# Kernel tuning notes

Hardware: AMD Instinct MI355X
Metric: run time of the kernel (lower is better)

## Reference

```python
import jax, jax.numpy as jnp
import numpy as np

NUM_EXPERTS = 8
TOP_K = 2
D = 1024


def setup_inputs() -> dict:
    key = jax.random.key(0)
    ks = jax.random.split(key, 5)
    T = 16384
    x = jax.random.normal(ks[0], (T, D), dtype=jnp.float32)
    # torch nn.Linear params: weight [out, in], bias [out]
    Wg = jax.random.normal(ks[1], (NUM_EXPERTS, D), dtype=jnp.float32) * (1.0 / np.sqrt(D))
    bg = jnp.zeros((NUM_EXPERTS,), dtype=jnp.float32)
    We = jax.random.normal(ks[2], (NUM_EXPERTS, D, D), dtype=jnp.float32) * (1.0 / np.sqrt(D))
    be = jax.random.normal(ks[3], (NUM_EXPERTS, D), dtype=jnp.float32) * 0.01
    return {"x": x, "Wg": Wg, "bg": bg, "We": We, "be": be}


def reference(x, Wg, bg, We, be):
    T = x.shape[0]
    # gate logits [T, E]
    gate_logits = x @ Wg.T + bg
    top_k_gates, top_k_idx = jax.lax.top_k(gate_logits, TOP_K)  # [T, K]
    top_k_gates = jax.nn.softmax(top_k_gates, axis=-1)
    # dense per-expert combine weight: sum of gate probs where idx == e
    combine = jnp.zeros((T, NUM_EXPERTS), dtype=x.dtype)
    combine = combine.at[jnp.arange(T)[:, None], top_k_idx].add(top_k_gates)  # [T, E]
    # all-expert dense matmul (faithful to the original naive loop): [E, T, out]
    expert_out = jnp.einsum('td,eod->eto', x, We) + be[:, None, :]
    # weighted combine: output[t] = sum_e combine[t,e] * expert_out[e,t]
    out = jnp.einsum('te,eto->to', combine, expert_out)
    return out
```

## Files before the change

kernel.cpp:

```cpp
#include <hip/hip_runtime.h>
#include <hip/hip_bf16.h>
#include <stdint.h>

#define DDIM 1024
#define NEXP 8
#define SEG  16384

typedef __attribute__((ext_vector_type(8))) short bf16x8;
typedef __attribute__((ext_vector_type(4))) float f32x4;
typedef __attribute__((ext_vector_type(8))) unsigned short u16x8;

__device__ __forceinline__ unsigned short f2bf(float f) {
    union { float f; unsigned int u; } v; v.f = f;
    unsigned int u = v.u;
    return (unsigned short)((u + 0x7FFFu + ((u >> 16) & 1u)) >> 16);
}
__device__ __forceinline__ float bf2f(unsigned short h) {
    union { unsigned int u; float f; } v; v.u = ((unsigned int)h) << 16;
    return v.f;
}

__global__ __launch_bounds__(512) void prep(
    const float* __restrict__ x, const float* __restrict__ Wg,
    const float* __restrict__ bg, const float* __restrict__ We,
    unsigned short* __restrict__ xb, unsigned short* __restrict__ web,
    int* __restrict__ cnt, int* __restrict__ tok_list,
    float* __restrict__ gate_list) {

    __shared__ int   se[64];
    __shared__ float sg[64];

    if (blockIdx.x >= 512) {
        size_t idx = ((size_t)(blockIdx.x - 512) * 512 + threadIdx.x) * 8;
        const f32x4* p = (const f32x4*)(We + idx);
        f32x4 a = __builtin_nontemporal_load(p);
        f32x4 b = __builtin_nontemporal_load(p + 1);
        u16x8 h;
        h[0] = f2bf(a[0]); h[1] = f2bf(a[1]); h[2] = f2bf(a[2]); h[3] = f2bf(a[3]);
        h[4] = f2bf(b[0]); h[5] = f2bf(b[1]); h[6] = f2bf(b[2]); h[7] = f2bf(b[3]);
        *(u16x8*)(web + idx) = h;
        return;
    }

    int wave = threadIdx.x >> 6, lane = threadIdx.x & 63;
    int tbase = blockIdx.x * 32;

#pragma unroll
    for (int i = 0; i < 4; i++) {
        int lt = wave * 4 + i;
        int t = tbase + lt;
        const float* xr = x + (size_t)t * DDIM;
        int c0 = lane * 16;

        float4 v[4];
#pragma unroll
        for (int j = 0; j < 4; j++) v[j] = ((const float4*)(xr + c0))[j];

        u16x8 h0, h1;
        h0[0] = f2bf(v[0].x); h0[1] = f2bf(v[0].y); h0[2] = f2bf(v[0].z); h0[3] = f2bf(v[0].w);
        h0[4] = f2bf(v[1].x); h0[5] = f2bf(v[1].y); h0[6] = f2bf(v[1].z); h0[7] = f2bf(v[1].w);
        h1[0] = f2bf(v[2].x); h1[1] = f2bf(v[2].y); h1[2] = f2bf(v[2].z); h1[3] = f2bf(v[2].w);
        h1[4] = f2bf(v[3].x); h1[5] = f2bf(v[3].y); h1[6] = f2bf(v[3].z); h1[7] = f2bf(v[3].w);
        u16x8* xo = (u16x8*)(xb + (size_t)t * DDIM + c0);
        xo[0] = h0; xo[1] = h1;

        float acc[NEXP];
#pragma unroll
        for (int e = 0; e < NEXP; e++) {
            const float4* wg = (const float4*)(Wg + e * DDIM + c0);
            float s = 0.f;
#pragma unroll
            for (int j = 0; j < 4; j++) {
                float4 w = wg[j];
                s += v[j].x * w.x + v[j].y * w.y + v[j].z * w.z + v[j].w * w.w;
            }
            acc[e] = s;
        }
#pragma unroll
        for (int e = 0; e < NEXP; e++) {
#pragma unroll
            for (int o = 32; o > 0; o >>= 1) acc[e] += __shfl_xor(acc[e], o, 64);
        }

        if (lane == 0) {
            float l1 = -1e30f, l2 = -1e30f; int e1 = 0, e2 = 0;
#pragma unroll
            for (int e = 0; e < NEXP; e++) {
                float le = acc[e] + bg[e];
                if (le > l1) { l2 = l1; e2 = e1; l1 = le; e1 = e; }
                else if (le > l2) { l2 = le; e2 = e; }
            }
            float g1 = 1.0f / (1.0f + __expf(l2 - l1));
            float g2 = 1.0f - g1;
            se[lt * 2]     = e1; sg[lt * 2]     = g1;
            se[lt * 2 + 1] = e2; sg[lt * 2 + 1] = g2;
        }
    }
    __syncthreads();

    if (threadIdx.x < NEXP) {
        int e = threadIdx.x;
        int k = 0;
#pragma unroll 8
        for (int i = 0; i < 64; i++) k += (se[i] == e);
        if (k) {
            int p = atomicAdd(cnt + e, k);
            for (int i = 0; i < 64; i++) {
                if (se[i] == e) {
                    tok_list[e * SEG + p]  = (tbase + (i >> 1)) * 2 + (i & 1);
                    gate_list[e * SEG + p] = sg[i];
                    p++;
                }
            }
        }
    }
}

template<bool STORE>
__global__ __launch_bounds__(256, 3) void moe_gemm(
    const unsigned short* __restrict__ xb, const unsigned short* __restrict__ web,
    const float* __restrict__ be, const int* __restrict__ cnt,
    const int* __restrict__ tok_list, const float* __restrict__ gate_list,
    unsigned short* __restrict__ Sb, float* __restrict__ outa) {

    int id = blockIdx.y, e = 0, c = 0;
    while (e < NEXP) {
        c = cnt[e];
        int mt = (c + 127) >> 7;
        if (id < mt) break;
        id -= mt; e++;
    }
    if (e == NEXP) return;
    int m0 = id << 7;
    int n0 = blockIdx.x << 7;

    __shared__ __align__(16) unsigned short lAB[16384];
    unsigned short* lA = lAB;
    unsigned short* lB = lAB + 8192;
    __shared__ int   tok_s[128];
    __shared__ float gate_s[128];

    int tid = threadIdx.x;
    int wave = tid >> 6, lane = tid & 63;

    if (tid < 128) {
        int r = m0 + tid;
        int rc = min(r, c - 1);
        tok_s[tid]  = tok_list[e * SEG + rc];
        gate_s[tid] = (r < c) ? gate_list[e * SEG + rc] : 0.0f;
    }
    __syncthreads();

    int rsub = lane >> 3;
    int gsrc = (lane & 7) ^ rsub;

    const unsigned short* agp[4];
    const unsigned short* bgp[4];
#pragma unroll
    for (int j = 0; j < 4; j++) {
        int row = (wave * 4 + j) * 8 + rsub;
        agp[j] = xb + (size_t)(tok_s[row] >> 1) * DDIM + gsrc * 8;
        bgp[j] = web + ((size_t)e << 20) + (size_t)(n0 + row) * DDIM + gsrc * 8;
    }

    f32x4 acc[4][4];
    f32x4 zz = {0.f, 0.f, 0.f, 0.f};
#pragma unroll
    for (int mi = 0; mi < 4; mi++)
#pragma unroll
        for (int ni = 0; ni < 4; ni++) acc[mi][ni] = zz;

    int wm = (wave >> 1) * 64;
    int wn = (wave & 1) * 64;
    int mrow = lane & 15;
    int q = lane >> 4;

    int offA[4], swA[4], offB[4], swB[4];
#pragma unroll
    for (int i = 0; i < 4; i++) {
        int ra = wm + i * 16 + mrow;
        offA[i] = ra * 64; swA[i] = ra & 7;
        int rb = wn + i * 16 + mrow;
        offB[i] = rb * 64; swB[i] = rb & 7;
    }

    for (int kt = 0; kt < 16; kt++) {
        int k0 = kt * 64;
#pragma unroll
        for (int j = 0; j < 4; j++) {
            __builtin_amdgcn_global_load_lds(
                (const __attribute__((address_space(1))) void*)(agp[j] + k0),
                (__attribute__((address_space(3))) void*)(&lA[(wave * 4 + j) * 512]),
                16, 0, 0);
            __builtin_amdgcn_global_load_lds(
                (const __attribute__((address_space(1))) void*)(bgp[j] + k0),
                (__attribute__((address_space(3))) void*)(&lB[(wave * 4 + j) * 512]),
                16, 0, 0);
        }
        __syncthreads();
#pragma unroll
        for (int kh = 0; kh < 2; kh++) {
            int gq = kh * 4 + q;
            bf16x8 af[4], bfr[4];
#pragma unroll
            for (int i = 0; i < 4; i++)
                af[i] = *(const bf16x8*)&lA[offA[i] + ((gq ^ swA[i]) << 3)];
#pragma unroll
            for (int i = 0; i < 4; i++)
                bfr[i] = *(const bf16x8*)&lB[offB[i] + ((gq ^ swB[i]) << 3)];
#pragma unroll
            for (int mi = 0; mi < 4; mi++)
#pragma unroll
                for (int ni = 0; ni < 4; ni++)
                    acc[mi][ni] = __builtin_amdgcn_mfma_f32_16x16x32_bf16(
                        af[mi], bfr[ni], acc[mi][ni], 0, 0, 0);
        }
        __syncthreads();
    }

    if (STORE) {
#pragma unroll
        for (int ni = 0; ni < 4; ni++) {
            int col = wn + ni * 16 + mrow;
            float bias = be[e * DDIM + n0 + col];
            int cg = col >> 3, cl = col & 7;
#pragma unroll
            for (int mi = 0; mi < 4; mi++) {
#pragma unroll
                for (int r = 0; r < 4; r++) {
                    int row = wm + mi * 16 + q * 4 + r;
                    float vv = gate_s[row] * (acc[mi][ni][r] + bias);
                    lAB[row * 128 + ((cg ^ (row & 7)) << 3) + cl] = f2bf(vv);
                }
            }
        }
        __syncthreads();
#pragma unroll
        for (int j = 0; j < 8; j++) {
            int t = j * 256 + tid;
            int row = t >> 4, gc = t & 15;
            u16x8 vv = *(const u16x8*)&lAB[row * 128 + ((gc ^ (row & 7)) << 3)];
            if (m0 + row < c)
                *(u16x8*)(Sb + (size_t)tok_s[row] * DDIM + n0 + gc * 8) = vv;
        }
    } else {
#pragma unroll
        for (int ni = 0; ni < 4; ni++) {
            int col = n0 + wn + ni * 16 + mrow;
            float bias = be[e * DDIM + col];
#pragma unroll
            for (int mi = 0; mi < 4; mi++) {
#pragma unroll
                for (int r = 0; r < 4; r++) {
                    int rl = wm + mi * 16 + q * 4 + r;
                    if (m0 + rl < c) {
                        float g = gate_s[rl];
                        atomicAdd(outa + (size_t)(tok_s[rl] >> 1) * DDIM + col,
                                  g * (acc[mi][ni][r] + bias));
                    }
                }
            }
        }
    }
}

__global__ void combine(const unsigned short* __restrict__ S, float* __restrict__ out) {
    size_t i = (size_t)blockIdx.x * 256 + threadIdx.x;
    size_t t = i >> 7;
    size_t g = i & 127;
    const u16x8* r0 = (const u16x8*)(S + t * 2 * DDIM) + g;
    const u16x8* r1 = (const u16x8*)(S + (t * 2 + 1) * DDIM) + g;
    u16x8 a = *r0;
    u16x8 b = *r1;
    f32x4 o0, o1;
#pragma unroll
    for (int k = 0; k < 4; k++) o0[k] = bf2f(a[k]) + bf2f(b[k]);
#pragma unroll
    for (int k = 0; k < 4; k++) o1[k] = bf2f(a[4 + k]) + bf2f(b[4 + k]);
    f32x4* op = (f32x4*)(out + t * DDIM + g * 8);
    __builtin_nontemporal_store(o0, op);
    __builtin_nontemporal_store(o1, op + 1);
}

extern "C" void kernel_launch(void* const* d_in, const int* in_sizes, int n_in,
                              void* d_out, int out_size, void* d_ws, size_t ws_size,
                              hipStream_t stream) {
    const float* x  = (const float*)d_in[0];
    const float* Wg = (const float*)d_in[1];
    const float* bg = (const float*)d_in[2];
    const float* We = (const float*)d_in[3];
    const float* be = (const float*)d_in[4];
    float* out = (float*)d_out;

    char* ws = (char*)d_ws;
    unsigned short* xb  = (unsigned short*)ws;
    unsigned short* web = (unsigned short*)(ws + 33554432);
    int*   tok_list  = (int*)(ws + 33554432 + 16777216);
    float* gate_list = (float*)(ws + 33554432 + 16777216 + 524288);
    int*   cnt       = (int*)(ws + 33554432 + 16777216 + 1048576);
    unsigned short* S = (unsigned short*)(ws + 52428800);

    const size_t NEED = 52428800ull + (size_t)32768 * DDIM * 2;

    hipMemsetAsync(cnt, 0, NEXP * sizeof(int), stream);

    prep<<<2560, 512, 0, stream>>>(x, Wg, bg, We, xb, web, cnt, tok_list, gate_list);

    if (ws_size >= NEED) {
        moe_gemm<true><<<dim3(8, 264), 256, 0, stream>>>(
            xb, web, be, cnt, tok_list, gate_list, S, nullptr);
        combine<<<8192, 256, 0, stream>>>(S, out);
    } else {
        hipMemsetAsync(d_out, 0, (size_t)out_size * sizeof(float), stream);
        moe_gemm<false><<<dim3(8, 264), 256, 0, stream>>>(
            xb, web, be, cnt, tok_list, gate_list, nullptr, out);
    }
}
```

Before: 306.1 us.

## Use 128x256 tiles with triple-buffered LDS pipeline in MoE GEMM

Reworks the expert GEMM to use 128x256 output tiles, with each wave computing 128x64, and K-steps of 32. A three-stage LDS ring buffer in dynamic shared memory lets global loads for step k+2 overlap the MFMA work on step k, synchronised by vmcnt waits and barriers instead of two __syncthreads per step. It also adds s_setprio around MFMAs and changes the prep kernel's x/Wg access to a half-row-split layout. The cost is more accumulator registers (occupancy bound drops from 3 to 2 blocks) and 72KB of LDS per block.

```diff
diff --git a/kernel.cpp b/kernel.cpp
--- a/kernel.cpp
+++ b/kernel.cpp
@@ -50,30 +50,33 @@
         int lt = wave * 4 + i;
         int t = tbase + lt;
         const float* xr = x + (size_t)t * DDIM;
-        int c0 = lane * 16;
-
-        float4 v[4];
-#pragma unroll
-        for (int j = 0; j < 4; j++) v[j] = ((const float4*)(xr + c0))[j];
+        int c0 = lane * 8;
+
+        float4 v0 = ((const float4*)(xr + c0))[0];
+        float4 v1 = ((const float4*)(xr + c0))[1];
+        float4 v2 = ((const float4*)(xr + c0 + 512))[0];
+        float4 v3 = ((const float4*)(xr + c0 + 512))[1];
 
         u16x8 h0, h1;
-        h0[0] = f2bf(v[0].x); h0[1] = f2bf(v[0].y); h0[2] = f2bf(v[0].z); h0[3] = f2bf(v[0].w);
-        h0[4] = f2bf(v[1].x); h0[5] = f2bf(v[1].y); h0[6] = f2bf(v[1].z); h0[7] = f2bf(v[1].w);
-        h1[0] = f2bf(v[2].x); h1[1] = f2bf(v[2].y); h1[2] = f2bf(v[2].z); h1[3] = f2bf(v[2].w);
-        h1[4] = f2bf(v[3].x); h1[5] = f2bf(v[3].y); h1[6] = f2bf(v[3].z); h1[7] = f2bf(v[3].w);
-        u16x8* xo = (u16x8*)(xb + (size_t)t * DDIM + c0);
-        xo[0] = h0; xo[1] = h1;
+        h0[0] = f2bf(v0.x); h0[1] = f2bf(v0.y); h0[2] = f2bf(v0.z); h0[3] = f2bf(v0.w);
+        h0[4] = f2bf(v1.x); h0[5] = f2bf(v1.y); h0[6] = f2bf(v1.z); h0[7] = f2bf(v1.w);
+        h1[0] = f2bf(v2.x); h1[1] = f2bf(v2.y); h1[2] = f2bf(v2.z); h1[3] = f2bf(v2.w);
+        h1[4] = f2bf(v3.x); h1[5] = f2bf(v3.y); h1[6] = f2bf(v3.z); h1[7] = f2bf(v3.w);
+        *(u16x8*)(xb + (size_t)t * DDIM + c0) = h0;
+        *(u16x8*)(xb + (size_t)t * DDIM + c0 + 512) = h1;
 
         float acc[NEXP];
 #pragma unroll
         for (int e = 0; e < NEXP; e++) {
-            const float4* wg = (const float4*)(Wg + e * DDIM + c0);
-            float s = 0.f;
-#pragma unroll
-            for (int j = 0; j < 4; j++) {
-                float4 w = wg[j];
-                s += v[j].x * w.x + v[j].y * w.y + v[j].z * w.z + v[j].w * w.w;
-            }
+            const float* wr = Wg + e * DDIM;
+            float4 w0 = ((const float4*)(wr + c0))[0];
+            float4 w1 = ((const float4*)(wr + c0))[1];
+            float4 w2 = ((const float4*)(wr + c0 + 512))[0];
+            float4 w3 = ((const float4*)(wr + c0 + 512))[1];
+            float s = v0.x*w0.x + v0.y*w0.y + v0.z*w0.z + v0.w*w0.w;
+            s += v1.x*w1.x + v1.y*w1.y + v1.z*w1.z + v1.w*w1.w;
+            s += v2.x*w2.x + v2.y*w2.y + v2.z*w2.z + v2.w*w2.w;
+            s += v3.x*w3.x + v3.y*w3.y + v3.z*w3.z + v3.w*w3.w;
             acc[e] = s;
         }
 #pragma unroll
@@ -116,12 +119,46 @@
     }
 }
 
+
+__device__ __forceinline__ void stage_tile(const unsigned short* const* sp,
+                                           unsigned short* lbase, int wave, int kt) {
+    int ko = kt << 5;
+#pragma unroll
+    for (int j = 0; j < 6; ++j) {
+        __builtin_amdgcn_global_load_lds(
+            (const __attribute__((address_space(1))) void*)(sp[j] + ko),
+            (__attribute__((address_space(3))) void*)(lbase + (wave * 6 + j) * 512),
+            16, 0, 0);
+    }
+}
+
+__device__ __forceinline__ void tile_mma(const unsigned short* ba, int aoff, int boff,
+                                         f32x4 (&acc)[8][4]) {
+    bf16x8 af[8], bf[4];
+#pragma unroll
+    for (int mi = 0; mi < 8; ++mi) af[mi] = *(const bf16x8*)(ba + aoff + mi * 512);
+#pragma unroll
+    for (int ni = 0; ni < 4; ++ni) bf[ni] = *(const bf16x8*)(ba + boff + ni * 512);
+    __builtin_amdgcn_s_setprio(1);
+#pragma unroll
+    for (int mi = 0; mi < 8; ++mi)
+#pragma unroll
+        for (int ni = 0; ni < 4; ++ni)
+            acc[mi][ni] = __builtin_amdgcn_mfma_f32_16x16x32_bf16(
+                af[mi], bf[ni], acc[mi][ni], 0, 0, 0);
+    __builtin_amdgcn_s_setprio(0);
+}
+
 template<bool STORE>
-__global__ __launch_bounds__(256, 3) void moe_gemm(
+__global__ __launch_bounds__(256, 2) void moe_gemm(
     const unsigned short* __restrict__ xb, const unsigned short* __restrict__ web,
     const float* __restrict__ be, const int* __restrict__ cnt,
     const int* __restrict__ tok_list, const float* __restrict__ gate_list,
     unsigned short* __restrict__ Sb, float* __restrict__ outa) {
+
+    extern __shared__ __align__(16) unsigned short lbuf[];
+    __shared__ int   tok_s[128];
+    __shared__ float gate_s[128];
 
     int id = blockIdx.y, e = 0, c = 0;
     while (e < NEXP) {
@@ -132,13 +169,7 @@
     }
     if (e == NEXP) return;
     int m0 = id << 7;
-    int n0 = blockIdx.x << 7;
-
-    __shared__ __align__(16) unsigned short lAB[16384];
-    unsigned short* lA = lAB;
-    unsigned short* lB = lAB + 8192;
-    __shared__ int   tok_s[128];
-    __shared__ float gate_s[128];
+    int n0 = blockIdx.x << 8;
 
     int tid = threadIdx.x;
     int wave = tid >> 6, lane = tid & 63;
@@ -151,113 +182,95 @@
     }
     __syncthreads();
 
-    int rsub = lane >> 3;
-    int gsrc = (lane & 7) ^ rsub;
-
-    const unsigned short* agp[4];
-    const unsigned short* bgp[4];
-#pragma unroll
-    for (int j = 0; j < 4; j++) {
-        int row = (wave * 4 + j) * 8 + rsub;
-        agp[j] = xb + (size_t)(tok_s[row] >> 1) * DDIM + gsrc * 8;
-        bgp[j] = web + ((size_t)e << 20) + (size_t)(n0 + row) * DDIM + gsrc * 8;
-    }
-
-    f32x4 acc[4][4];
+    int g0 = ((lane & 3) - ((lane >> 3) & 3)) & 3;
+    const unsigned short* sp[6];
+#pragma unroll
+    for (int j = 0; j < 6; ++j) {
+        int ch = wave * 6 + j;
+        int sub = lane >> 2;
+        int arow = min((ch << 4) + sub, 127);
+        int brow = ((ch - 8) << 4) + sub;
+        const unsigned short* pa = xb + (size_t)(tok_s[arow] >> 1) * DDIM + g0 * 8;
+        const unsigned short* pb = web + ((size_t)e << 20) +
+                                   (size_t)(n0 + brow) * DDIM + g0 * 8;
+        sp[j] = (ch < 8) ? pa : pb;
+    }
+
+    int mrow = lane & 15, q = lane >> 4;
+    int ksl  = ((q + (mrow >> 1)) & 3) << 3;
+    int aoff = mrow * 32 + ksl;
+    int boff = 4096 + wave * 2048 + mrow * 32 + ksl;
+
+    f32x4 acc[8][4];
     f32x4 zz = {0.f, 0.f, 0.f, 0.f};
 #pragma unroll
-    for (int mi = 0; mi < 4; mi++)
-#pragma unroll
-        for (int ni = 0; ni < 4; ni++) acc[mi][ni] = zz;
-
-    int wm = (wave >> 1) * 64;
-    int wn = (wave & 1) * 64;
-    int mrow = lane & 15;
-    int q = lane >> 4;
-
-    int offA[4], swA[4], offB[4], swB[4];
-#pragma unroll
-    for (int i = 0; i < 4; i++) {
-        int ra = wm + i * 16 + mrow;
-        offA[i] = ra * 64; swA[i] = ra & 7;
-        int rb = wn + i * 16 + mrow;
-        offB[i] = rb * 64; swB[i] = rb & 7;
-    }
-
-    for (int kt = 0; kt < 16; kt++) {
-        int k0 = kt * 64;
-#pragma unroll
-        for (int j = 0; j < 4; j++) {
-            __builtin_amdgcn_global_load_lds(
-                (const __attribute__((address_space(1))) void*)(agp[j] + k0),
-                (__attribute__((address_space(3))) void*)(&lA[(wave * 4 + j) * 512]),
-                16, 0, 0);
-            __builtin_amdgcn_global_load_lds(
-                (const __attribute__((address_space(1))) void*)(bgp[j] + k0),
-                (__attribute__((address_space(3))) void*)(&lB[(wave * 4 + j) * 512]),
-                16, 0, 0);
-        }
+    for (int mi = 0; mi < 8; ++mi)
+#pragma unroll
+        for (int ni = 0; ni < 4; ++ni) acc[mi][ni] = zz;
+
+    stage_tile(sp, lbuf,         wave, 0);
+    stage_tile(sp, lbuf + 12288, wave, 1);
+
+    for (int kb = 0; kb < 10; ++kb) {
+#pragma unroll
+        for (int u = 0; u < 3; ++u) {
+            int kt = kb * 3 + u;
+            asm volatile("s_waitcnt vmcnt(6)" ::: "memory");
+            __builtin_amdgcn_s_barrier();
+            asm volatile("" ::: "memory");
+            stage_tile(sp, lbuf + ((u + 2) % 3) * 12288, wave, kt + 2);
+            tile_mma(lbuf + u * 12288, aoff, boff, acc);
+        }
+    }
+    asm volatile("s_waitcnt vmcnt(6)" ::: "memory");
+    __builtin_amdgcn_s_barrier();
+    asm volatile("" ::: "memory");
+    tile_mma(lbuf, aoff, boff, acc);
+
+    asm volatile("s_waitcnt vmcnt(0)" ::: "memory");
+    __builtin_amdgcn_s_barrier();
+    asm volatile("" ::: "memory");
+    tile_mma(lbuf + 12288, aoff, boff, acc);
+
+    if (STORE) {
         __syncthreads();
 #pragma unroll
-        for (int kh = 0; kh < 2; kh++) {
-            int gq = kh * 4 + q;
-            bf16x8 af[4], bfr[4];
-#pragma unroll
-            for (int i = 0; i < 4; i++)
-                af[i] = *(const bf16x8*)&lA[offA[i] + ((gq ^ swA[i]) << 3)];
-#pragma unroll
-            for (int i = 0; i < 4; i++)
-                bfr[i] = *(const bf16x8*)&lB[offB[i] + ((gq ^ swB[i]) << 3)];
-#pragma unroll
-            for (int mi = 0; mi < 4; mi++)
-#pragma unroll
-                for (int ni = 0; ni < 4; ni++)
-                    acc[mi][ni] = __builtin_amdgcn_mfma_f32_16x16x32_bf16(
-                        af[mi], bfr[ni], acc[mi][ni], 0, 0, 0);
-        }
-        __syncthreads();
-    }
-
-    if (STORE) {
-#pragma unroll
-        for (int ni = 0; ni < 4; ni++) {
-            int col = wn + ni * 16 + mrow;
+        for (int ni = 0; ni < 4; ++ni) {
+            int col = wave * 64 + ni * 16 + mrow;
             float bias = be[e * DDIM + n0 + col];
             int cg = col >> 3, cl = col & 7;
 #pragma unroll
-            for (int mi = 0; mi < 4; mi++) {
-#pragma unroll
-                for (int r = 0; r < 4; r++) {
-                    int row = wm + mi * 16 + q * 4 + r;
+            for (int mi = 0; mi < 8; ++mi) {
+#pragma unroll
+                for (int r = 0; r < 4; ++r) {
+                    int row = mi * 16 + q * 4 + r;
                     float vv = gate_s[row] * (acc[mi][ni][r] + bias);
-                    lAB[row * 128 + ((cg ^ (row & 7)) << 3) + cl] = f2bf(vv);
+                    lbuf[row * 256 + ((cg ^ (row & 7)) << 3) + cl] = f2bf(vv);
                 }
             }
         }
         __syncthreads();
 #pragma unroll
-        for (int j = 0; j < 8; j++) {
+        for (int j = 0; j < 16; ++j) {
             int t = j * 256 + tid;
-            int row = t >> 4, gc = t & 15;
-            u16x8 vv = *(const u16x8*)&lAB[row * 128 + ((gc ^ (row & 7)) << 3)];
+            int row = t >> 5, gc = t & 31;
+            u16x8 vv = *(const u16x8*)&lbuf[row * 256 + ((gc ^ (row & 7)) << 3)];
             if (m0 + row < c)
                 *(u16x8*)(Sb + (size_t)tok_s[row] * DDIM + n0 + gc * 8) = vv;
         }
     } else {
 #pragma unroll
-        for (int ni = 0; ni < 4; ni++) {
-            int col = n0 + wn + ni * 16 + mrow;
+        for (int ni = 0; ni < 4; ++ni) {
+            int col = n0 + wave * 64 + ni * 16 + mrow;
             float bias = be[e * DDIM + col];
 #pragma unroll
-            for (int mi = 0; mi < 4; mi++) {
-#pragma unroll
-                for (int r = 0; r < 4; r++) {
-                    int rl = wm + mi * 16 + q * 4 + r;
-                    if (m0 + rl < c) {
-                        float g = gate_s[rl];
+            for (int mi = 0; mi < 8; ++mi) {
+#pragma unroll
+                for (int r = 0; r < 4; ++r) {
+                    int rl = mi * 16 + q * 4 + r;
+                    if (m0 + rl < c)
                         atomicAdd(outa + (size_t)(tok_s[rl] >> 1) * DDIM + col,
-                                  g * (acc[mi][ni][r] + bias));
-                    }
+                                  gate_s[rl] * (acc[mi][ni][r] + bias));
                 }
             }
         }
@@ -302,17 +315,26 @@
 
     const size_t NEED = 52428800ull + (size_t)32768 * DDIM * 2;
 
+    static bool attr_done = false;
+    if (!attr_done) {
+        hipFuncSetAttribute(reinterpret_cast<const void*>(moe_gemm<true>),
+                            hipFuncAttributeMaxDynamicSharedMemorySize, 73728);
+        hipFuncSetAttribute(reinterpret_cast<const void*>(moe_gemm<false>),
+                            hipFuncAttributeMaxDynamicSharedMemorySize, 73728);
+        attr_done = true;
+    }
+
     hipMemsetAsync(cnt, 0, NEXP * sizeof(int), stream);
 
     prep<<<2560, 512, 0, stream>>>(x, Wg, bg, We, xb, web, cnt, tok_list, gate_list);
 
     if (ws_size >= NEED) {
-        moe_gemm<true><<<dim3(8, 264), 256, 0, stream>>>(
+        moe_gemm<true><<<dim3(4, 264), 256, 73728, stream>>>(
             xb, web, be, cnt, tok_list, gate_list, S, nullptr);
         combine<<<8192, 256, 0, stream>>>(S, out);
     } else {
         hipMemsetAsync(d_out, 0, (size_t)out_size * sizeof(float), stream);
-        moe_gemm<false><<<dim3(8, 264), 256, 0, stream>>>(
+        moe_gemm<false><<<dim3(4, 264), 256, 73728, stream>>>(
             xb, web, be, cnt, tok_list, gate_list, nullptr, out);
     }
 }
```

Result: faster. 276.6 us (-9.6%).
